# Optimization experiments

Measured on AMD Instinct MI355X. Metric: run time of the kernel, lower is better.

Reference implementation:

```python
import jax, jax.numpy as jnp
import numpy as np

V, E, H, T = 50000, 300, 512, 16   # vocab, embed_dim, hidden_dim, tagset
Hh = H // 2                         # per-direction LSTM hidden
B, S = 128, 128                     # batch (hardcoded in module), seq_len
START, STOP = 14, 15
NEG = -10000.0


def setup_inputs() -> dict:
    key = jax.random.key(0)
    ks = jax.random.split(key, 16)
    n = lambda k, sh: (jax.random.normal(k, sh, dtype=jnp.float32) * 0.1)
    trans = jax.random.normal(ks[12], (T, T), dtype=jnp.float32)
    trans = trans.at[START, :].set(NEG).at[:, STOP].set(NEG)
    return {
        "sentence": jax.random.randint(ks[0], (B, S), 0, V, dtype=jnp.int32),
        "emb": jax.random.normal(ks[1], (V, E), dtype=jnp.float32),
        "Wih_f": n(ks[2], (4 * Hh, E)), "Whh_f": n(ks[3], (4 * Hh, Hh)),
        "bih_f": n(ks[4], (4 * Hh,)),   "bhh_f": n(ks[5], (4 * Hh,)),
        "Wih_b": n(ks[6], (4 * Hh, E)), "Whh_b": n(ks[7], (4 * Hh, Hh)),
        "bih_b": n(ks[8], (4 * Hh,)),   "bhh_b": n(ks[9], (4 * Hh,)),
        "W_out": n(ks[10], (T, H)),     "b_out": n(ks[11], (T,)),
        "trans": trans,
        "h0": jax.random.normal(ks[13], (2, B, Hh), dtype=jnp.float32),
        "c0": jax.random.normal(ks[14], (2, B, Hh), dtype=jnp.float32),
    }


def _lstm_dir(x_sbE, h0, c0, Wih, Whh, bih, bhh):
    """x_sbE: [S,B,E] -> [S,B,Hh]. PyTorch gate order: i,f,g,o."""
    def cell(carry, xt):
        h, c = carry
        g = xt @ Wih.T + bih + h @ Whh.T + bhh
        i, f, gg, o = jnp.split(g, 4, axis=-1)
        c = jax.nn.sigmoid(f) * c + jax.nn.sigmoid(i) * jnp.tanh(gg)
        h = jax.nn.sigmoid(o) * jnp.tanh(c)
        return (h, c), h
    _, hs = jax.lax.scan(cell, (h0, c0), x_sbE)
    return hs


def _viterbi(feats, trans):
    """Batched Viterbi. feats: [B,S,T]. Returns (scores [B], paths [B,S])."""
    init = jnp.full((B, T), NEG, dtype=feats.dtype).at[:, START].set(0.0)

    def step(fv, feat_t):
        # next_tag_var[b, next, prev] = fv[b, prev] + trans[next, prev]
        nxt = fv[:, None, :] + trans[None, :, :]
        bp = jnp.argmax(nxt, axis=-1)              # [B,T]
        fv = jnp.max(nxt, axis=-1) + feat_t        # [B,T]
        return fv, bp

    fv, bps = jax.lax.scan(step, init, jnp.swapaxes(feats, 0, 1))  # bps: [S,B,T]
    term = fv + trans[STOP][None, :]
    best = jnp.argmax(term, axis=-1)               # [B]
    score = jnp.max(term, axis=-1)                 # [B]

    def back(tag, bp_t):
        prev = jnp.take_along_axis(bp_t, tag[:, None], axis=1)[:, 0]
        return prev, tag

    _, path = jax.lax.scan(back, best, bps, reverse=True)  # [S,B]
    return score, jnp.swapaxes(path, 0, 1)


def reference(sentence, emb, Wih_f, Whh_f, bih_f, bhh_f,
              Wih_b, Whh_b, bih_b, bhh_b, W_out, b_out, trans, h0, c0):
    x = emb[sentence]                               # [B,S,E] (frozen embedding)
    x_sbE = jnp.swapaxes(x, 0, 1)                   # [S,B,E]
    h_f = _lstm_dir(x_sbE, h0[0], c0[0], Wih_f, Whh_f, bih_f, bhh_f)
    h_b = _lstm_dir(x_sbE[::-1], h0[1], c0[1], Wih_b, Whh_b, bih_b, bhh_b)[::-1]
    lstm_out = jnp.concatenate([h_f, h_b], axis=-1)  # [S,B,H]
    feats = jnp.swapaxes(lstm_out @ W_out.T + b_out, 0, 1)  # [B,S,T]
    scores, tag_seqs = _viterbi(feats, trans)
    return scores, tag_seqs
```

## Files before the change

### kernel.cpp

```cpp
#include <hip/hip_runtime.h>
#include <math.h>
#include <stdint.h>

#define BB 128
#define SS 128
#define EE 300
#define HH 256
#define G4 1024
#define TT 16
#define NEGV -10000.0f
#define START_TAG 14
#define STOP_TAG 15

typedef float f32x4 __attribute__((ext_vector_type(4)));

__device__ __forceinline__ float sigm(float x) { return 1.0f / (1.0f + expf(-x)); }

__device__ __forceinline__ float4 shfl_xor4(float4 v, int m) {
  float4 r;
  r.x = __shfl_xor(v.x, m); r.y = __shfl_xor(v.y, m);
  r.z = __shfl_xor(v.z, m); r.w = __shfl_xor(v.w, m);
  return r;
}
__device__ __forceinline__ void add4(float4& a, const float4& b) {
  a.x += b.x; a.y += b.y; a.z += b.z; a.w += b.w;
}

__device__ __forceinline__ void load_pairs16(const float* p, f32x4& a, f32x4& b,
                                             f32x4& c, f32x4& d) {
  asm volatile("global_load_dwordx4 %0, %4, off sc0 sc1\n\t"
               "global_load_dwordx4 %1, %4, off offset:16 sc0 sc1\n\t"
               "global_load_dwordx4 %2, %4, off offset:32 sc0 sc1\n\t"
               "global_load_dwordx4 %3, %4, off offset:48 sc0 sc1\n\t"
               "s_waitcnt vmcnt(0)"
               : "=&v"(a), "=&v"(b), "=&v"(c), "=&v"(d) : "v"(p) : "memory");
}

__device__ __forceinline__ void store_pair_llc(float2* p, float h, int stamp) {
  uint64_t bits = ((uint64_t)(uint32_t)stamp << 32) | (uint64_t)__float_as_uint(h);
  __hip_atomic_store((uint64_t*)p, bits, __ATOMIC_RELAXED, __HIP_MEMORY_SCOPE_AGENT);
}

__global__ void k_prep(const float* __restrict__ Wih_f, const float* __restrict__ Whh_f,
                       const float* __restrict__ bih_f, const float* __restrict__ bhh_f,
                       const float* __restrict__ Wih_b, const float* __restrict__ Whh_b,
                       const float* __restrict__ bih_b, const float* __restrict__ bhh_b,
                       float* __restrict__ WihT, float* __restrict__ Whh4,
                       float* __restrict__ bsum) {
  int id = blockIdx.x * blockDim.x + threadIdx.x;
  const int N1 = 2 * EE * G4;
  const int N2 = 2 * HH * G4;
  const int N3 = 2 * G4;
  if (id < N1) {
    int d = id / (EE * G4); int r = id % (EE * G4);
    int e = r / G4; int j = r % G4;
    const float* W = d ? Wih_b : Wih_f;
    WihT[id] = W[j * EE + e];
  } else if (id < N1 + N2) {
    int t = id - N1;
    int d = t / (HH * G4); int r = t % (HH * G4);
    int k = r / G4; int q = r % G4; int u = q >> 2; int g = q & 3;
    const float* W = d ? Whh_b : Whh_f;
    Whh4[t] = W[(g * HH + u) * HH + k];
  } else if (id < N1 + N2 + N3) {
    int t = id - N1 - N2;
    int d = t / G4; int j = t % G4;
    bsum[t] = d ? (bih_b[j] + bhh_b[j]) : (bih_f[j] + bhh_f[j]);
  }
}

__global__ void k_xproj(const int* __restrict__ sent, const float* __restrict__ emb,
                        const float* __restrict__ WihT, const float* __restrict__ bsum,
                        float4* __restrict__ xp4) {
  __shared__ float xs[16][EE];
  __shared__ int idxs[16];
  int blk = blockIdx.x;
  int d = blk >> 10;
  int tile = blk & 1023;
  int tid = threadIdx.x;
  if (tid < 16) {
    int sb = tile * 16 + tid;
    int s = sb >> 7, b = sb & 127;
    idxs[tid] = sent[b * SS + s];
  }
  __syncthreads();
  for (int t = tid; t < 16 * EE; t += 256) {
    int i = t / EE, e = t % EE;
    xs[i][e] = emb[(size_t)idxs[i] * EE + e];
  }
  __syncthreads();

  const float* WT = WihT + (size_t)d * EE * G4;
  float acc0[16], acc1[16], acc2[16], acc3[16];
#pragma unroll
  for (int i = 0; i < 16; ++i) { acc0[i] = 0.f; acc1[i] = 0.f; acc2[i] = 0.f; acc3[i] = 0.f; }

  for (int e = 0; e < EE; ++e) {
    const float* row = WT + (size_t)e * G4;
    float w0 = row[tid];
    float w1 = row[tid + 256];
    float w2 = row[tid + 512];
    float w3 = row[tid + 768];
#pragma unroll
    for (int i = 0; i < 16; ++i) {
      float x = xs[i][e];
      acc0[i] += w0 * x; acc1[i] += w1 * x; acc2[i] += w2 * x; acc3[i] += w3 * x;
    }
  }
  float b0 = bsum[d * G4 + tid];
  float b1 = bsum[d * G4 + tid + 256];
  float b2 = bsum[d * G4 + tid + 512];
  float b3 = bsum[d * G4 + tid + 768];
#pragma unroll
  for (int i = 0; i < 16; ++i) {
    int sb = tile * 16 + i;
    int s = sb >> 7, b = sb & 127;
    xp4[(((size_t)d * SS + s) * BB + b) * HH + tid] =
        make_float4(acc0[i] + b0, acc1[i] + b1, acc2[i] + b2, acc3[i] + b3);
  }
}

__global__ __launch_bounds__(256, 1) void k_recur(
    const float4* __restrict__ xp4, const float4* __restrict__ Wg,
    const float* __restrict__ Wout, const float* __restrict__ h0,
    const float* __restrict__ c0, float2* __restrict__ hpair,
    float* __restrict__ featsP) {
  __shared__ __align__(16) float hsh[2][8 * 288];
  __shared__ float hloc[2][8 * 33];
  __shared__ float WoL[16 * 33];

  int blk = blockIdx.x;
  int d = blk >> 7;
  int bg = (blk >> 3) & 15;
  int sl = blk & 7;
  int bbase = bg * 8;
  int tid = threadIdx.x;
  int u = tid >> 3, kc = tid & 7;
  int uglob = sl * 32 + u;

  for (int i = tid; i < 16 * 32; i += 256) {
    int t = i >> 5, uu = i & 31;
    WoL[t * 33 + uu] = Wout[t * 512 + d * HH + sl * 32 + uu];
  }

  float4 wreg[32];
  {
    const float4* Wd = Wg + (size_t)d * (HH * HH) + (size_t)(kc * 32) * HH + uglob;
#pragma unroll
    for (int kk = 0; kk < 32; ++kk) wreg[kk] = Wd[(size_t)kk * HH];
  }
  int b_own = ((kc & 1) << 2) | (kc & 2) | ((kc >> 2) & 1);
  float c_reg = c0[((size_t)d * BB + bbase + b_own) * HH + uglob];
  bool up0 = (kc & 1), up1 = (kc & 2), up2 = (kc & 4);

  int sb = tid >> 5;
  int sk = (tid & 31) * 8;
  int ldoff = sb * 288 + (sk >> 5) * 36 + (sk & 31);

  for (int step = 0; step < SS; ++step) {
    int s = d ? (SS - 1 - step) : step;
    int pb = step & 1;
    float4 xg = xp4[(((size_t)d * SS + s) * BB + bbase + b_own) * HH + uglob];

    float* ldst = &hsh[pb][ldoff];
    if (step == 0) {
      const float* ps = h0 + ((size_t)d * BB + bbase) * HH + (tid << 3);
      *(f32x4*)ldst = *(const f32x4*)ps;
      *(f32x4*)(ldst + 4) = *(const f32x4*)(ps + 4);
    } else {
      int slot_r = (step + 2) % 3;
      const float* ps = (const float*)(hpair +
          ((size_t)(slot_r * 2 + d) * BB + bbase + sb) * HH + sk);
      f32x4 p0, p1, p2, p3;
      for (;;) {
        load_pairs16(ps, p0, p1, p2, p3);
        if (__float_as_int(p0[1]) == step && __float_as_int(p0[3]) == step &&
            __float_as_int(p1[1]) == step && __float_as_int(p1[3]) == step &&
            __float_as_int(p2[1]) == step && __float_as_int(p2[3]) == step &&
            __float_as_int(p3[1]) == step && __float_as_int(p3[3]) == step)
          break;
      }
      f32x4 lo, hi;
      lo[0] = p0[0]; lo[1] = p0[2]; lo[2] = p1[0]; lo[3] = p1[2];
      hi[0] = p2[0]; hi[1] = p2[2]; hi[2] = p3[0]; hi[3] = p3[2];
      *(f32x4*)ldst = lo;
      *(f32x4*)(ldst + 4) = hi;
    }
    __syncthreads();

    if (step > 0) {
      int b2 = tid >> 5, t = (tid >> 1) & 15, pr = tid & 1;
      int s_prev = d ? (SS - step) : (step - 1);
      float p = 0.f;
#pragma unroll
      for (int q = 0; q < 16; ++q)
        p += hloc[1 - pb][b2 * 33 + pr * 16 + q] * WoL[t * 33 + pr * 16 + q];
      p += __shfl_xor(p, 1);
      if (!pr)
        featsP[(((size_t)(d * 8 + sl) * BB + bbase + b2) * SS + s_prev) * TT + t] = p;
    }

    const float* hb = &hsh[pb][0];
    float4 a[8];
#pragma unroll
    for (int b = 0; b < 8; ++b) a[b] = make_float4(0.f, 0.f, 0.f, 0.f);
#pragma unroll
    for (int kk4 = 0; kk4 < 8; ++kk4) {
      float hvv[8][4];
#pragma unroll
      for (int b = 0; b < 8; ++b)
        *(f32x4*)&hvv[b][0] = *(const f32x4*)&hb[b * 288 + kc * 36 + kk4 * 4];
#pragma unroll
      for (int j = 0; j < 4; ++j) {
        float4 w = wreg[kk4 * 4 + j];
#pragma unroll
        for (int b = 0; b < 8; ++b) {
          float hj = hvv[b][j];
          a[b].x += w.x * hj; a[b].y += w.y * hj;
          a[b].z += w.z * hj; a[b].w += w.w * hj;
        }
      }
    }

#pragma unroll
    for (int j = 0; j < 4; ++j) {
      float4 snd = up0 ? a[j] : a[j + 4];
      float4 rcv = shfl_xor4(snd, 1);
      if (!up0) add4(a[j], rcv); else add4(a[j + 4], rcv);
    }
    float4 v0 = up0 ? a[4] : a[0];
    float4 v1 = up0 ? a[5] : a[1];
    float4 v2 = up0 ? a[6] : a[2];
    float4 v3 = up0 ? a[7] : a[3];
    {
      float4 snd = up1 ? v0 : v2;
      float4 rcv = shfl_xor4(snd, 2);
      if (!up1) add4(v0, rcv); else add4(v2, rcv);
      snd = up1 ? v1 : v3;
      rcv = shfl_xor4(snd, 2);
      if (!up1) add4(v1, rcv); else add4(v3, rcv);
    }
    float4 w0 = up1 ? v2 : v0;
    float4 w1 = up1 ? v3 : v1;
    {
      float4 snd = up2 ? w0 : w1;
      float4 rcv = shfl_xor4(snd, 4);
      if (!up2) add4(w0, rcv); else add4(w1, rcv);
    }
    float4 g4 = up2 ? w1 : w0;

    float ii = g4.x + xg.x, ff = g4.y + xg.y, gg = g4.z + xg.z, oo = g4.w + xg.w;
    c_reg = sigm(ff) * c_reg + sigm(ii) * tanhf(gg);
    float hn = sigm(oo) * tanhf(c_reg);

    store_pair_llc(&hpair[((size_t)((step % 3) * 2 + d) * BB + bbase + b_own) * HH + uglob],
                   hn, step + 1);
    hloc[pb][b_own * 33 + u] = hn;
  }

  __syncthreads();
  {
    int b2 = tid >> 5, t = (tid >> 1) & 15, pr = tid & 1;
    int s_prev = d ? 0 : (SS - 1);
    float p = 0.f;
#pragma unroll
    for (int q = 0; q < 16; ++q)
      p += hloc[1][b2 * 33 + pr * 16 + q] * WoL[t * 33 + pr * 16 + q];
    p += __shfl_xor(p, 1);
    if (!pr)
      featsP[(((size_t)(d * 8 + sl) * BB + bbase + b2) * SS + s_prev) * TT + t] = p;
  }
}

__global__ void k_fsum(const float* __restrict__ featsP, float* __restrict__ featsF) {
  int b = blockIdx.x;
  int tid = threadIdx.x;
  float acc[8];
#pragma unroll
  for (int j = 0; j < 8; ++j) acc[j] = 0.f;
  for (int dsl = 0; dsl < 16; ++dsl) {
    const float* fp = featsP + ((size_t)dsl * BB + b) * (SS * TT);
#pragma unroll
    for (int j = 0; j < 8; ++j) acc[j] += fp[j * 256 + tid];
  }
  float* fo = featsF + (size_t)b * (SS * TT);
#pragma unroll
  for (int j = 0; j < 8; ++j) fo[j * 256 + tid] = acc[j];
}

__global__ void k_viterbi(const float* __restrict__ featsF, const float* __restrict__ b_out,
                          const float* __restrict__ trans, float* __restrict__ out) {
  __shared__ float tr[TT * TT];
  __shared__ unsigned char bpl[16][SS][TT];
  int tid = threadIdx.x;
  if (tid < TT * TT) tr[tid] = trans[tid];
  __syncthreads();

  int bg = tid >> 4;
  int next = tid & 15;
  int b = blockIdx.x * 16 + bg;
  float fv = (next == START_TAG) ? 0.0f : NEGV;
  float bo = b_out[next];
  const float* fF = featsF + (size_t)b * SS * TT;

  for (int s = 0; s < SS; ++s) {
    float best = -INFINITY; int arg = 0;
#pragma unroll
    for (int prev = 0; prev < TT; ++prev) {
      float fvp = __shfl(fv, prev, 16);
      float cand = fvp + tr[next * TT + prev];
      if (cand > best) { best = cand; arg = prev; }
    }
    float feat = fF[s * TT + next] + bo;
    fv = best + feat;
    bpl[bg][s][next] = (unsigned char)arg;
  }

  float bv = fv + tr[STOP_TAG * TT + next];
  int bi = next;
#pragma unroll
  for (int off = 8; off; off >>= 1) {
    float ov = __shfl_down(bv, off, 16);
    int oi = __shfl_down(bi, off, 16);
    if (ov > bv || (ov == bv && oi < bi)) { bv = ov; bi = oi; }
  }
  if (next == 0) {
    out[b] = bv;
    int tag = bi;
    float* po = out + BB + (size_t)b * SS;
    for (int s = SS - 1; s >= 0; --s) {
      po[s] = (float)tag;
      tag = bpl[bg][s][tag];
    }
  }
}

extern "C" void kernel_launch(void* const* d_in, const int* in_sizes, int n_in,
                              void* d_out, int out_size, void* d_ws, size_t ws_size,
                              hipStream_t stream) {
  const int*   sent  = (const int*)d_in[0];
  const float* emb   = (const float*)d_in[1];
  const float* Wih_f = (const float*)d_in[2];
  const float* Whh_f = (const float*)d_in[3];
  const float* bih_f = (const float*)d_in[4];
  const float* bhh_f = (const float*)d_in[5];
  const float* Wih_b = (const float*)d_in[6];
  const float* Whh_b = (const float*)d_in[7];
  const float* bih_b = (const float*)d_in[8];
  const float* bhh_b = (const float*)d_in[9];
  const float* Wout  = (const float*)d_in[10];
  const float* b_out = (const float*)d_in[11];
  const float* trans = (const float*)d_in[12];
  const float* h0    = (const float*)d_in[13];
  const float* c0    = (const float*)d_in[14];

  float* ws = (float*)d_ws;
  size_t off = 0;
  float* xproj  = ws + off; off += (size_t)2 * SS * BB * G4;
  float* WihT   = ws + off; off += (size_t)2 * EE * G4;
  float* Whh4   = ws + off; off += (size_t)2 * HH * G4;
  float* bsum   = ws + off; off += (size_t)2 * G4;
  float* featsP = ws + off; off += (size_t)16 * BB * SS * TT;
  float* featsF = ws + off; off += (size_t)BB * SS * TT;
  float* hpairf = ws + off; off += (size_t)3 * 2 * BB * HH * 2;

  const int NPREP = 2 * EE * G4 + 2 * HH * G4 + 2 * G4;
  k_prep<<<(NPREP + 255) / 256, 256, 0, stream>>>(Wih_f, Whh_f, bih_f, bhh_f,
                                                  Wih_b, Whh_b, bih_b, bhh_b,
                                                  WihT, Whh4, bsum);
  k_xproj<<<2048, 256, 0, stream>>>(sent, emb, WihT, bsum, (float4*)xproj);

  {
    const float4* xp4c = (const float4*)xproj;
    const float4* Wgc  = (const float4*)Whh4;
    float2* hpair = (float2*)hpairf;
    void* kargs[] = {(void*)&xp4c, (void*)&Wgc, (void*)&Wout, (void*)&h0,
                     (void*)&c0, (void*)&hpair, (void*)&featsP};
    hipError_t e = hipLaunchCooperativeKernel(k_recur, dim3(256), dim3(256),
                                              kargs, 0, stream);
    if (e != hipSuccess) {
      k_recur<<<256, 256, 0, stream>>>(xp4c, Wgc, Wout, h0, c0, hpair, featsP);
    }
  }

  k_fsum<<<BB, 256, 0, stream>>>(featsP, featsF);
  k_viterbi<<<8, 256, 0, stream>>>(featsF, b_out, trans, (float*)d_out);
}
```

Baseline: 945.3 us.

## Vectorize xproj loads and use block-wide ballot polling in LSTM recurrence

The input projection kernel now gathers embedding rows and reads shared x values as 4-wide vectors, which cuts the number of load instructions. The recurrence kernel replaces per-thread spin loops with a block-wide vote (ballot plus shared flags and a barrier) and an s_sleep between polls. The per-step output projection is moved after the poll, so it runs before the h staging writes. This lowers memory-polling pressure but adds a barrier to every poll iteration, and the reordering depends on the double buffering of hloc staying correct.

```diff
diff --git a/kernel.cpp b/kernel.cpp
--- a/kernel.cpp
+++ b/kernel.cpp
@@ -72,7 +72,7 @@
 __global__ void k_xproj(const int* __restrict__ sent, const float* __restrict__ emb,
                         const float* __restrict__ WihT, const float* __restrict__ bsum,
                         float4* __restrict__ xp4) {
-  __shared__ float xs[16][EE];
+  __shared__ __align__(16) float xs[16][EE];
   __shared__ int idxs[16];
   int blk = blockIdx.x;
   int d = blk >> 10;
@@ -84,9 +84,9 @@
     idxs[tid] = sent[b * SS + s];
   }
   __syncthreads();
-  for (int t = tid; t < 16 * EE; t += 256) {
-    int i = t / EE, e = t % EE;
-    xs[i][e] = emb[(size_t)idxs[i] * EE + e];
+  for (int t = tid; t < 16 * 75; t += 256) {
+    int i = t / 75, e4 = t % 75;
+    ((f32x4*)&xs[i][0])[e4] = ((const f32x4*)(emb + (size_t)idxs[i] * EE))[e4];
   }
   __syncthreads();
 
@@ -95,16 +95,24 @@
 #pragma unroll
   for (int i = 0; i < 16; ++i) { acc0[i] = 0.f; acc1[i] = 0.f; acc2[i] = 0.f; acc3[i] = 0.f; }
 
-  for (int e = 0; e < EE; ++e) {
-    const float* row = WT + (size_t)e * G4;
-    float w0 = row[tid];
-    float w1 = row[tid + 256];
-    float w2 = row[tid + 512];
-    float w3 = row[tid + 768];
-#pragma unroll
-    for (int i = 0; i < 16; ++i) {
-      float x = xs[i][e];
-      acc0[i] += w0 * x; acc1[i] += w1 * x; acc2[i] += w2 * x; acc3[i] += w3 * x;
+  for (int e4 = 0; e4 < 75; ++e4) {
+    f32x4 xv[16];
+#pragma unroll
+    for (int i = 0; i < 16; ++i)
+      xv[i] = *(const f32x4*)&xs[i][e4 * 4];
+    const float* rowb = WT + (size_t)e4 * 4 * G4;
+#pragma unroll
+    for (int j = 0; j < 4; ++j) {
+      const float* row = rowb + (size_t)j * G4;
+      float w0 = row[tid];
+      float w1 = row[tid + 256];
+      float w2 = row[tid + 512];
+      float w3 = row[tid + 768];
+#pragma unroll
+      for (int i = 0; i < 16; ++i) {
+        float x = xv[i][j];
+        acc0[i] += w0 * x; acc1[i] += w1 * x; acc2[i] += w2 * x; acc3[i] += w3 * x;
+      }
     }
   }
   float b0 = bsum[d * G4 + tid];
@@ -128,6 +136,7 @@
   __shared__ __align__(16) float hsh[2][8 * 288];
   __shared__ float hloc[2][8 * 33];
   __shared__ float WoL[16 * 33];
+  __shared__ int vflag[4];
 
   int blk = blockIdx.x;
   int d = blk >> 7;
@@ -167,37 +176,44 @@
       const float* ps = h0 + ((size_t)d * BB + bbase) * HH + (tid << 3);
       *(f32x4*)ldst = *(const f32x4*)ps;
       *(f32x4*)(ldst + 4) = *(const f32x4*)(ps + 4);
+      __syncthreads();
     } else {
       int slot_r = (step + 2) % 3;
       const float* ps = (const float*)(hpair +
           ((size_t)(slot_r * 2 + d) * BB + bbase + sb) * HH + sk);
       f32x4 p0, p1, p2, p3;
+      load_pairs16(ps, p0, p1, p2, p3);
       for (;;) {
+        bool ok = (__float_as_int(p0[1]) == step && __float_as_int(p0[3]) == step &&
+                   __float_as_int(p1[1]) == step && __float_as_int(p1[3]) == step &&
+                   __float_as_int(p2[1]) == step && __float_as_int(p2[3]) == step &&
+                   __float_as_int(p3[1]) == step && __float_as_int(p3[3]) == step);
+        unsigned long long bl = __ballot(ok);
+        if ((tid & 63) == 0) vflag[tid >> 6] = (bl == ~0ull);
+        __syncthreads();
+        bool good = vflag[0] && vflag[1] && vflag[2] && vflag[3];
+        if (good) break;
+        __builtin_amdgcn_s_sleep(2);
         load_pairs16(ps, p0, p1, p2, p3);
-        if (__float_as_int(p0[1]) == step && __float_as_int(p0[3]) == step &&
-            __float_as_int(p1[1]) == step && __float_as_int(p1[3]) == step &&
-            __float_as_int(p2[1]) == step && __float_as_int(p2[3]) == step &&
-            __float_as_int(p3[1]) == step && __float_as_int(p3[3]) == step)
-          break;
+        __syncthreads();
+      }
+      {
+        int b2 = tid >> 5, t = (tid >> 1) & 15, pr = tid & 1;
+        int s_prev = d ? (SS - step) : (step - 1);
+        float p = 0.f;
+#pragma unroll
+        for (int q = 0; q < 16; ++q)
+          p += hloc[1 - pb][b2 * 33 + pr * 16 + q] * WoL[t * 33 + pr * 16 + q];
+        p += __shfl_xor(p, 1);
+        if (!pr)
+          featsP[(((size_t)(d * 8 + sl) * BB + bbase + b2) * SS + s_prev) * TT + t] = p;
       }
       f32x4 lo, hi;
       lo[0] = p0[0]; lo[1] = p0[2]; lo[2] = p1[0]; lo[3] = p1[2];
       hi[0] = p2[0]; hi[1] = p2[2]; hi[2] = p3[0]; hi[3] = p3[2];
       *(f32x4*)ldst = lo;
       *(f32x4*)(ldst + 4) = hi;
-    }
-    __syncthreads();
-
-    if (step > 0) {
-      int b2 = tid >> 5, t = (tid >> 1) & 15, pr = tid & 1;
-      int s_prev = d ? (SS - step) : (step - 1);
-      float p = 0.f;
-#pragma unroll
-      for (int q = 0; q < 16; ++q)
-        p += hloc[1 - pb][b2 * 33 + pr * 16 + q] * WoL[t * 33 + pr * 16 + q];
-      p += __shfl_xor(p, 1);
-      if (!pr)
-        featsP[(((size_t)(d * 8 + sl) * BB + bbase + b2) * SS + s_prev) * TT + t] = p;
+      __syncthreads();
     }
 
     const float* hb = &hsh[pb][0];
```

After: 1.093 ms. 15.6% more time.
